# Kernel tuning notes

Hardware: AMD Instinct MI355X
Metric: run time of the kernel (lower is better)

The kernel has to match this reference:

```python
import jax, jax.numpy as jnp
import numpy as np

DIM = 1024
HIDDEN = 2816  # multiple_of * ceil(int(2*4096/3)/multiple_of)
N_MODALITIES = 2
B, S = 8, 4096


def setup_inputs() -> dict:
    key = jax.random.key(0)
    k_x, k_m, k1, k2, k3 = jax.random.split(key, 5)
    x = jax.random.normal(k_x, (B, S, DIM), dtype=jnp.float32)
    modality_ids = jax.random.randint(k_m, (B, S), 0, N_MODALITIES, dtype=jnp.int32)
    in_std = DIM ** -0.5
    out_std = HIDDEN ** -0.5
    # Linear weight layout: [out_features, in_features], stacked over modalities.
    W1 = jax.random.normal(k1, (N_MODALITIES, HIDDEN, DIM), dtype=jnp.float32) * in_std
    W3 = jax.random.normal(k3, (N_MODALITIES, HIDDEN, DIM), dtype=jnp.float32) * in_std
    W2 = jax.random.normal(k2, (N_MODALITIES, DIM, HIDDEN), dtype=jnp.float32) * out_std
    return {"x": x, "modality_ids": modality_ids, "W1": W1, "W2": W2, "W3": W3}


def reference(x, modality_ids, W1, W2, W3):
    # Masked per-modality SwiGLU; equivalent to gather -> expert MLP -> scatter.
    output = jnp.zeros_like(x)
    for m in range(N_MODALITIES):  # small fixed modality count
        mask = (modality_ids == m)[..., None]          # [B, S, 1]
        x1 = jnp.einsum('bsd,hd->bsh', x, W1[m])       # gate proj
        x3 = jnp.einsum('bsd,hd->bsh', x, W3[m])       # up proj
        out_m = jnp.einsum('bsh,dh->bsd', jax.nn.silu(x1) * x3, W2[m])
        output = output + jnp.where(mask, out_m, 0.0)
    return output
```

## Files before the change

kernel.cpp:

```cpp
#include <hip/hip_runtime.h>
#include <stdint.h>

#define DIMK 1024
#define HID  2816

typedef __attribute__((ext_vector_type(8))) __bf16 bf16x8;
typedef __attribute__((ext_vector_type(4))) float  f32x4;

typedef const __attribute__((address_space(1))) void* gas1_t;
typedef __attribute__((address_space(3))) void*       las3_t;

__device__ __forceinline__ uint16_t f2bf(float f) {
  uint32_t u = __float_as_uint(f);
  u += 0x7FFFu + ((u >> 16) & 1u);
  return (uint16_t)(u >> 16);
}

__device__ __forceinline__ void gload16(const uint16_t* g, uint16_t* l) {
  __builtin_amdgcn_global_load_lds((gas1_t)g, (las3_t)l, 16, 0, 0);
}

template<int N> __device__ __forceinline__ void wait_vm() {
  if constexpr (N == 0)      asm volatile("s_waitcnt vmcnt(0)" ::: "memory");
  else if constexpr (N == 2) asm volatile("s_waitcnt vmcnt(2)" ::: "memory");
  else                       asm volatile("s_waitcnt vmcnt(4)" ::: "memory");
}

__device__ __forceinline__ void stage_half(const uint16_t* g, long stride,
                                           uint16_t* lds, int wv, int lane) {
  const int rsub = lane >> 3;
  const int gsw  = ((lane & 7) ^ rsub) << 3;
#pragma unroll
  for (int j = 0; j < 2; ++j) {
    const int blk = j * 8 + wv;
    gload16(g + (long)(blk * 8 + rsub) * stride + gsw,
            lds + blk * 512 + lane * 8);
  }
}

__device__ __forceinline__ bf16x8 ldsf(const uint16_t* lds, int r, int g) {
  return *reinterpret_cast<const bf16x8*>(lds + r * 64 + ((g ^ (r & 7)) << 3));
}


__global__ void count_kernel(const int* __restrict__ mids, int* __restrict__ bc, int T) {
  const int b = blockIdx.x, t = threadIdx.x;
  const int token = b * 256 + t;
  const int lane = t & 63, wv = t >> 6;
  const int m = (token < T) ? mids[token] : -1;
  unsigned long long m0 = __ballot(m == 0);
  unsigned long long m1 = __ballot(m == 1);
  __shared__ int w0[4], w1[4];
  if (lane == 0) { w0[wv] = __popcll(m0); w1[wv] = __popcll(m1); }
  __syncthreads();
  if (t == 0) {
    bc[2 * b]     = w0[0] + w0[1] + w0[2] + w0[3];
    bc[2 * b + 1] = w1[0] + w1[1] + w1[2] + w1[3];
  }
}

__global__ void scan_kernel(const int* __restrict__ bc, int* __restrict__ base,
                            int* __restrict__ counters, int nb) {
  __shared__ int s0[256], s1[256];
  const int t = threadIdx.x;
  const int v0 = (t < nb) ? bc[2 * t] : 0;
  const int v1 = (t < nb) ? bc[2 * t + 1] : 0;
  s0[t] = v0; s1[t] = v1;
  __syncthreads();
  for (int off = 1; off < 256; off <<= 1) {
    int a0 = (t >= off) ? s0[t - off] : 0;
    int a1 = (t >= off) ? s1[t - off] : 0;
    __syncthreads();
    s0[t] += a0; s1[t] += a1;
    __syncthreads();
  }
  if (t < nb) { base[2 * t] = s0[t] - v0; base[2 * t + 1] = s1[t] - v1; }
  if (t == nb - 1) { counters[0] = s0[t]; counters[1] = s1[t]; }
}

__global__ void slot_kernel(const int* __restrict__ mids, const int* __restrict__ base,
                            const int* __restrict__ counters, int* __restrict__ tok,
                            int* __restrict__ slotof, int T) {
  const int b = blockIdx.x, t = threadIdx.x;
  const int token = b * 256 + t;
  const int lane = t & 63, wv = t >> 6;
  const int m = (token < T) ? mids[token] : -1;
  unsigned long long m0 = __ballot(m == 0);
  unsigned long long m1 = __ballot(m == 1);
  __shared__ int w0[4], w1[4];
  if (lane == 0) { w0[wv] = __popcll(m0); w1[wv] = __popcll(m1); }
  __syncthreads();
  int pre0 = 0, pre1 = 0;
  for (int w = 0; w < wv; ++w) { pre0 += w0[w]; pre1 += w1[w]; }
  if (token >= T) return;
  const unsigned long long below = (1ULL << lane) - 1ULL;
  const int c0 = counters[0];
  const int al0 = ((c0 + 255) >> 8) << 8;
  int slot;
  if (m == 0) slot = base[2 * b] + pre0 + __popcll(m0 & below);
  else        slot = al0 + base[2 * b + 1] + pre1 + __popcll(m1 & below);
  tok[slot] = token;
  slotof[token] = slot;
}

__global__ void copy_kernel(const float* __restrict__ x, const int* __restrict__ slotof,
                            uint16_t* __restrict__ xg, int T) {
  const int token = blockIdx.x * 4 + (threadIdx.x >> 6);
  if (token >= T) return;
  const int lane = threadIdx.x & 63;
  const int slot = slotof[token];
  const float4* src = (const float4*)(x + (long)token * DIMK);
  uint16_t* dst = xg + (long)slot * DIMK;
#pragma unroll
  for (int j = 0; j < 4; ++j) {
    float4 v = src[lane + 64 * j];
    ushort4 o;
    o.x = f2bf(v.x); o.y = f2bf(v.y); o.z = f2bf(v.z); o.w = f2bf(v.w);
    *(ushort4*)(dst + (lane + 64 * j) * 4) = o;
  }
}

__global__ void convert_kernel(const float* __restrict__ src, uint16_t* __restrict__ dst, long n) {
  long i = ((long)blockIdx.x * blockDim.x + threadIdx.x) * 4;
  if (i >= n) return;
  float4 v = *(const float4*)(src + i);
  ushort4 o;
  o.x = f2bf(v.x); o.y = f2bf(v.y); o.z = f2bf(v.z); o.w = f2bf(v.w);
  *(ushort4*)(dst + i) = o;
}


template<bool PF, int W0, int W1, int W2>
__device__ __forceinline__ void g1_tile(
    const uint16_t* Ac, const uint16_t* B1c, const uint16_t* B3c,
    uint16_t* An, uint16_t* B1n, uint16_t* B3n,
    const uint16_t* gA, const uint16_t* gB1, const uint16_t* gB3, long ko,
    int wv, int lane, int wr, int wc, int lrow, int grp,
    f32x4 (&accG)[8][2], f32x4 (&accU)[8][2]) {
  bf16x8 a[4][2], b1[2][2], b3[2][2];
  wait_vm<W0>();
  __builtin_amdgcn_s_barrier();
  asm volatile("" ::: "memory");
#pragma unroll
  for (int m = 0; m < 4; ++m)
#pragma unroll
    for (int ks = 0; ks < 2; ++ks)
      a[m][ks] = ldsf(Ac, m * 32 + wr * 16 + lrow, ks * 4 + grp);
#pragma unroll
  for (int n = 0; n < 2; ++n)
#pragma unroll
    for (int ks = 0; ks < 2; ++ks)
      b1[n][ks] = ldsf(B1c, wc * 32 + n * 16 + lrow, ks * 4 + grp);
  if constexpr (PF) stage_half(gA + ko, DIMK, An, wv, lane);
  asm volatile("s_waitcnt lgkmcnt(0)" ::: "memory");
  __builtin_amdgcn_sched_barrier(0);
  __builtin_amdgcn_s_setprio(1);
#pragma unroll
  for (int ks = 0; ks < 2; ++ks)
#pragma unroll
    for (int m = 0; m < 4; ++m)
#pragma unroll
      for (int n = 0; n < 2; ++n)
        accG[m][n] = __builtin_amdgcn_mfma_f32_16x16x32_bf16(a[m][ks], b1[n][ks], accG[m][n], 0, 0, 0);
  __builtin_amdgcn_s_setprio(0);
  wait_vm<W1>();
  __builtin_amdgcn_s_barrier();
  asm volatile("" ::: "memory");
#pragma unroll
  for (int n = 0; n < 2; ++n)
#pragma unroll
    for (int ks = 0; ks < 2; ++ks)
      b3[n][ks] = ldsf(B3c, wc * 32 + n * 16 + lrow, ks * 4 + grp);
  if constexpr (PF) stage_half(gB1 + ko, DIMK, B1n, wv, lane);
  asm volatile("s_waitcnt lgkmcnt(0)" ::: "memory");
  __builtin_amdgcn_sched_barrier(0);
  __builtin_amdgcn_s_setprio(1);
#pragma unroll
  for (int ks = 0; ks < 2; ++ks)
#pragma unroll
    for (int m = 0; m < 4; ++m)
#pragma unroll
      for (int n = 0; n < 2; ++n)
        accU[m][n] = __builtin_amdgcn_mfma_f32_16x16x32_bf16(a[m][ks], b3[n][ks], accU[m][n], 0, 0, 0);
  __builtin_amdgcn_s_setprio(0);
  wait_vm<W2>();
  __builtin_amdgcn_s_barrier();
  asm volatile("" ::: "memory");
#pragma unroll
  for (int m = 0; m < 4; ++m)
#pragma unroll
    for (int ks = 0; ks < 2; ++ks)
      a[m][ks] = ldsf(Ac, (m + 4) * 32 + wr * 16 + lrow, ks * 4 + grp);
  if constexpr (PF) stage_half(gB3 + ko, DIMK, B3n, wv, lane);
  asm volatile("s_waitcnt lgkmcnt(0)" ::: "memory");
  __builtin_amdgcn_sched_barrier(0);
  __builtin_amdgcn_s_setprio(1);
#pragma unroll
  for (int ks = 0; ks < 2; ++ks)
#pragma unroll
    for (int m = 0; m < 4; ++m)
#pragma unroll
      for (int n = 0; n < 2; ++n)
        accG[m + 4][n] = __builtin_amdgcn_mfma_f32_16x16x32_bf16(a[m][ks], b1[n][ks], accG[m + 4][n], 0, 0, 0);
  __builtin_amdgcn_s_setprio(0);
  if constexpr (PF) stage_half(gA + 128 * DIMK + ko, DIMK, An + 128 * 64, wv, lane);
  __builtin_amdgcn_s_setprio(1);
#pragma unroll
  for (int ks = 0; ks < 2; ++ks)
#pragma unroll
    for (int m = 0; m < 4; ++m)
#pragma unroll
      for (int n = 0; n < 2; ++n)
        accU[m + 4][n] = __builtin_amdgcn_mfma_f32_16x16x32_bf16(a[m][ks], b3[n][ks], accU[m + 4][n], 0, 0, 0);
  __builtin_amdgcn_s_setprio(0);
}

__global__ __launch_bounds__(512, 2) void gemm1_kernel(
    const uint16_t* __restrict__ xg, const uint16_t* __restrict__ w1b,
    const uint16_t* __restrict__ w3b, uint16_t* __restrict__ hbuf,
    const int* __restrict__ counters) {
  __shared__ __align__(16) uint16_t lsA[2][256 * 64];
  __shared__ __align__(16) uint16_t lsB1[2][128 * 64];
  __shared__ __align__(16) uint16_t lsB3[2][128 * 64];

  const int c0 = counters[0], c1 = counters[1];
  const int t0 = (c0 + 255) >> 8, t1 = (c1 + 255) >> 8;
  const int GX = gridDim.x;
  const int nwg = GX * (int)gridDim.y;
  const int orig = blockIdx.y * GX + blockIdx.x;
  const int q = nwg >> 3, r = nwg & 7;
  const int xcd = orig & 7, loc = orig >> 3;
  const int swz = (xcd < r ? xcd * (q + 1) : r * (q + 1) + (xcd - r) * q) + loc;
  const int ht = swz / GX;
  const int rt = swz - ht * GX;
  if (rt >= t0 + t1) return;
  const int mod = (rt < t0) ? 0 : 1;
  const long row0 = (long)rt * 256;

  const int tid = threadIdx.x, lane = tid & 63, wv = tid >> 6;
  const int wr = wv >> 2, wc = wv & 3;
  const int lrow = lane & 15, grp = lane >> 4;

  const uint16_t* gA  = xg  + row0 * DIMK;
  const uint16_t* gB1 = w1b + ((long)mod * HID + ht * 128) * DIMK;
  const uint16_t* gB3 = w3b + ((long)mod * HID + ht * 128) * DIMK;

  f32x4 accG[8][2], accU[8][2];
#pragma unroll
  for (int m = 0; m < 8; ++m)
#pragma unroll
    for (int n = 0; n < 2; ++n) {
      accG[m][n] = {0.f, 0.f, 0.f, 0.f};
      accU[m][n] = {0.f, 0.f, 0.f, 0.f};
    }

  stage_half(gA,             DIMK, &lsA[0][0],        wv, lane);
  stage_half(gB1,            DIMK, &lsB1[0][0],       wv, lane);
  stage_half(gB3,            DIMK, &lsB3[0][0],       wv, lane);
  stage_half(gA + 128 * DIMK, DIMK, &lsA[0][128 * 64], wv, lane);

  const int NT = DIMK / 64;
  int cur = 0;
  for (int t = 0; t < NT - 1; ++t) {
    g1_tile<true, 4, 4, 4>(&lsA[cur][0], &lsB1[cur][0], &lsB3[cur][0],
                           &lsA[cur ^ 1][0], &lsB1[cur ^ 1][0], &lsB3[cur ^ 1][0],
                           gA, gB1, gB3, (long)(t + 1) * 64,
                           wv, lane, wr, wc, lrow, grp, accG, accU);
    cur ^= 1;
  }
  g1_tile<false, 4, 2, 0>(&lsA[cur][0], &lsB1[cur][0], &lsB3[cur][0],
                          &lsA[cur ^ 1][0], &lsB1[cur ^ 1][0], &lsB3[cur ^ 1][0],
                          gA, gB1, gB3, 0,
                          wv, lane, wr, wc, lrow, grp, accG, accU);

#pragma unroll
  for (int m = 0; m < 8; ++m)
#pragma unroll
    for (int n = 0; n < 2; ++n) {
      const int col = ht * 128 + wc * 32 + n * 16 + lrow;
#pragma unroll
      for (int i = 0; i < 4; ++i) {
        const long row = row0 + m * 32 + wr * 16 + grp * 4 + i;
        float g = accG[m][n][i];
        float u = accU[m][n][i];
        float hv = (g / (1.f + __expf(-g))) * u;
        hbuf[row * HID + col] = f2bf(hv);
      }
    }
}


template<bool PF, int W0, int W1>
__device__ __forceinline__ void g2_tile(
    const uint16_t* Ac, const uint16_t* Bc, uint16_t* An, uint16_t* Bn,
    const uint16_t* gA, const uint16_t* gB, long ko,
    int wv, int lane, int wr, int wc, int lrow, int grp,
    f32x4 (&acc)[8][2]) {
  bf16x8 a[4][2], b[2][2];
  wait_vm<W0>();
  __builtin_amdgcn_s_barrier();
  asm volatile("" ::: "memory");
#pragma unroll
  for (int m = 0; m < 4; ++m)
#pragma unroll
    for (int ks = 0; ks < 2; ++ks)
      a[m][ks] = ldsf(Ac, m * 32 + wr * 16 + lrow, ks * 4 + grp);
#pragma unroll
  for (int n = 0; n < 2; ++n)
#pragma unroll
    for (int ks = 0; ks < 2; ++ks)
      b[n][ks] = ldsf(Bc, wc * 32 + n * 16 + lrow, ks * 4 + grp);
  if constexpr (PF) {
    stage_half(gA + ko, HID, An, wv, lane);
    stage_half(gB + ko, HID, Bn, wv, lane);
  }
  asm volatile("s_waitcnt lgkmcnt(0)" ::: "memory");
  __builtin_amdgcn_sched_barrier(0);
  __builtin_amdgcn_s_setprio(1);
#pragma unroll
  for (int ks = 0; ks < 2; ++ks)
#pragma unroll
    for (int m = 0; m < 4; ++m)
#pragma unroll
      for (int n = 0; n < 2; ++n)
        acc[m][n] = __builtin_amdgcn_mfma_f32_16x16x32_bf16(a[m][ks], b[n][ks], acc[m][n], 0, 0, 0);
  __builtin_amdgcn_s_setprio(0);
  wait_vm<W1>();
  __builtin_amdgcn_s_barrier();
  asm volatile("" ::: "memory");
#pragma unroll
  for (int m = 0; m < 4; ++m)
#pragma unroll
    for (int ks = 0; ks < 2; ++ks)
      a[m][ks] = ldsf(Ac, (m + 4) * 32 + wr * 16 + lrow, ks * 4 + grp);
  if constexpr (PF) stage_half(gA + 128 * HID + ko, HID, An + 128 * 64, wv, lane);
  asm volatile("s_waitcnt lgkmcnt(0)" ::: "memory");
  __builtin_amdgcn_sched_barrier(0);
  __builtin_amdgcn_s_setprio(1);
#pragma unroll
  for (int ks = 0; ks < 2; ++ks)
#pragma unroll
    for (int m = 0; m < 4; ++m)
#pragma unroll
      for (int n = 0; n < 2; ++n)
        acc[m + 4][n] = __builtin_amdgcn_mfma_f32_16x16x32_bf16(a[m][ks], b[n][ks], acc[m + 4][n], 0, 0, 0);
  __builtin_amdgcn_s_setprio(0);
}

__global__ __launch_bounds__(512, 2) void gemm2_kernel(
    const uint16_t* __restrict__ hbuf, const uint16_t* __restrict__ w2b,
    const int* __restrict__ counters, const int* __restrict__ tok,
    float* __restrict__ out) {
  __shared__ __align__(16) uint16_t lsA[2][256 * 64];
  __shared__ __align__(16) uint16_t lsB[2][128 * 64];

  const int c0 = counters[0], c1 = counters[1];
  const int t0 = (c0 + 255) >> 8, t1 = (c1 + 255) >> 8;
  const int GX = gridDim.x;
  const int nwg = GX * (int)gridDim.y;
  const int orig = blockIdx.y * GX + blockIdx.x;
  const int q = nwg >> 3, r = nwg & 7;
  const int xcd = orig & 7, loc = orig >> 3;
  const int swz = (xcd < r ? xcd * (q + 1) : r * (q + 1) + (xcd - r) * q) + loc;
  const int ct = swz / GX;
  const int rt = swz - ct * GX;
  if (rt >= t0 + t1) return;
  const int mod = (rt < t0) ? 0 : 1;
  const long row0 = (long)rt * 256;
  const int vlimit = (mod == 0) ? c0 : t0 * 256 + c1;

  const int tid = threadIdx.x, lane = tid & 63, wv = tid >> 6;
  const int wr = wv >> 2, wc = wv & 3;
  const int lrow = lane & 15, grp = lane >> 4;

  const uint16_t* gA = hbuf + row0 * HID;
  const uint16_t* gB = w2b + ((long)mod * DIMK + ct * 128) * HID;

  f32x4 acc[8][2];
#pragma unroll
  for (int m = 0; m < 8; ++m)
#pragma unroll
    for (int n = 0; n < 2; ++n) acc[m][n] = {0.f, 0.f, 0.f, 0.f};

  stage_half(gA,             HID, &lsA[0][0],        wv, lane);
  stage_half(gB,             HID, &lsB[0][0],        wv, lane);
  stage_half(gA + 128 * HID, HID, &lsA[0][128 * 64], wv, lane);

  const int NT = HID / 64;
  int cur = 0;
  for (int t = 0; t < NT - 1; ++t) {
    g2_tile<true, 2, 4>(&lsA[cur][0], &lsB[cur][0],
                        &lsA[cur ^ 1][0], &lsB[cur ^ 1][0],
                        gA, gB, (long)(t + 1) * 64,
                        wv, lane, wr, wc, lrow, grp, acc);
    cur ^= 1;
  }
  g2_tile<false, 2, 0>(&lsA[cur][0], &lsB[cur][0],
                       &lsA[cur ^ 1][0], &lsB[cur ^ 1][0],
                       gA, gB, 0,
                       wv, lane, wr, wc, lrow, grp, acc);

#pragma unroll
  for (int m = 0; m < 8; ++m)
#pragma unroll
    for (int n = 0; n < 2; ++n) {
      const int col = ct * 128 + wc * 32 + n * 16 + lrow;
#pragma unroll
      for (int i = 0; i < 4; ++i) {
        const int row = (int)row0 + m * 32 + wr * 16 + grp * 4 + i;
        if (row < vlimit) {
          out[(long)tok[row] * DIMK + col] = acc[m][n][i];
        }
      }
    }
}

extern "C" void kernel_launch(void* const* d_in, const int* in_sizes, int n_in,
                              void* d_out, int out_size, void* d_ws, size_t ws_size,
                              hipStream_t stream) {
  const float* x    = (const float*)d_in[0];
  const int*   mids = (const int*)d_in[1];
  const float* W1   = (const float*)d_in[2];
  const float* W2   = (const float*)d_in[3];
  const float* W3   = (const float*)d_in[4];
  float* out = (float*)d_out;

  const int T   = in_sizes[1];
  const int NB  = (T + 255) / 256;
  const int CAP = ((T + 255) & ~255) + 256;

  char* ws = (char*)d_ws;
  int* counters = (int*)ws;
  int* bc   = (int*)(ws + 256);
  int* base = (int*)(ws + 256 + 2048);
  int* tok  = (int*)(ws + 256 + 4096);
  int* slotof = tok + ((CAP + 63) & ~63);
  size_t off = 256 + 4096 + (size_t)((CAP + 63) & ~63) * 4 + (size_t)((T + 63) & ~63) * 4;
  off = (off + 255) & ~(size_t)255;
  uint16_t* xg  = (uint16_t*)(ws + off); off += (size_t)CAP * DIMK * 2;
  uint16_t* w1b = (uint16_t*)(ws + off); off += (size_t)2 * HID * DIMK * 2;
  uint16_t* w3b = (uint16_t*)(ws + off); off += (size_t)2 * HID * DIMK * 2;
  uint16_t* w2b = (uint16_t*)(ws + off); off += (size_t)2 * DIMK * HID * 2;
  uint16_t* hbuf = (uint16_t*)(ws + off); off += (size_t)CAP * HID * 2;
  (void)ws_size; (void)n_in; (void)out_size;

  count_kernel<<<NB, 256, 0, stream>>>(mids, bc, T);
  scan_kernel<<<1, 256, 0, stream>>>(bc, base, counters, NB);
  slot_kernel<<<NB, 256, 0, stream>>>(mids, base, counters, tok, slotof, T);
  copy_kernel<<<(T + 3) / 4, 256, 0, stream>>>(x, slotof, xg, T);

  const long NW = (long)2 * HID * DIMK;
  const int cblk = (int)((NW / 4 + 255) / 256);
  convert_kernel<<<cblk, 256, 0, stream>>>(W1, w1b, NW);
  convert_kernel<<<cblk, 256, 0, stream>>>(W3, w3b, NW);
  convert_kernel<<<cblk, 256, 0, stream>>>(W2, w2b, NW);

  const int rtiles = CAP / 256;
  gemm1_kernel<<<dim3(rtiles, HID / 128), 512, 0, stream>>>(xg, w1b, w3b, hbuf, counters);
  gemm2_kernel<<<dim3(rtiles, DIMK / 128), 512, 0, stream>>>(hbuf, w2b, counters, tok, out);
}
```

Baseline: 772.9 us.

## Widen gemm2 tile to 256 columns and restructure both GEMM inner pipelines

```diff
diff --git a/kernel.cpp b/kernel.cpp
--- a/kernel.cpp
+++ b/kernel.cpp
@@ -23,7 +23,7 @@
 template<int N> __device__ __forceinline__ void wait_vm() {
   if constexpr (N == 0)      asm volatile("s_waitcnt vmcnt(0)" ::: "memory");
   else if constexpr (N == 2) asm volatile("s_waitcnt vmcnt(2)" ::: "memory");
-  else                       asm volatile("s_waitcnt vmcnt(4)" ::: "memory");
+  else                       asm volatile("s_waitcnt vmcnt(6)" ::: "memory");
 }
 
 __device__ __forceinline__ void stage_half(const uint16_t* g, long stride,
@@ -130,7 +130,7 @@
 }
 
 
-template<bool PF, int W0, int W1, int W2>
+template<bool PF, int W0, int W2>
 __device__ __forceinline__ void g1_tile(
     const uint16_t* Ac, const uint16_t* B1c, const uint16_t* B3c,
     uint16_t* An, uint16_t* B1n, uint16_t* B3n,
@@ -143,75 +143,78 @@
   asm volatile("" ::: "memory");
 #pragma unroll
   for (int m = 0; m < 4; ++m)
-#pragma unroll
-    for (int ks = 0; ks < 2; ++ks)
-      a[m][ks] = ldsf(Ac, m * 32 + wr * 16 + lrow, ks * 4 + grp);
-#pragma unroll
-  for (int n = 0; n < 2; ++n)
-#pragma unroll
-    for (int ks = 0; ks < 2; ++ks)
-      b1[n][ks] = ldsf(B1c, wc * 32 + n * 16 + lrow, ks * 4 + grp);
-  if constexpr (PF) stage_half(gA + ko, DIMK, An, wv, lane);
-  asm volatile("s_waitcnt lgkmcnt(0)" ::: "memory");
-  __builtin_amdgcn_sched_barrier(0);
-  __builtin_amdgcn_s_setprio(1);
-#pragma unroll
-  for (int ks = 0; ks < 2; ++ks)
-#pragma unroll
-    for (int m = 0; m < 4; ++m)
-#pragma unroll
-      for (int n = 0; n < 2; ++n)
-        accG[m][n] = __builtin_amdgcn_mfma_f32_16x16x32_bf16(a[m][ks], b1[n][ks], accG[m][n], 0, 0, 0);
-  __builtin_amdgcn_s_setprio(0);
-  wait_vm<W1>();
-  __builtin_amdgcn_s_barrier();
-  asm volatile("" ::: "memory");
-#pragma unroll
-  for (int n = 0; n < 2; ++n)
-#pragma unroll
-    for (int ks = 0; ks < 2; ++ks)
-      b3[n][ks] = ldsf(B3c, wc * 32 + n * 16 + lrow, ks * 4 + grp);
-  if constexpr (PF) stage_half(gB1 + ko, DIMK, B1n, wv, lane);
-  asm volatile("s_waitcnt lgkmcnt(0)" ::: "memory");
-  __builtin_amdgcn_sched_barrier(0);
-  __builtin_amdgcn_s_setprio(1);
-#pragma unroll
-  for (int ks = 0; ks < 2; ++ks)
-#pragma unroll
-    for (int m = 0; m < 4; ++m)
-#pragma unroll
-      for (int n = 0; n < 2; ++n)
-        accU[m][n] = __builtin_amdgcn_mfma_f32_16x16x32_bf16(a[m][ks], b3[n][ks], accU[m][n], 0, 0, 0);
+    a[m][0] = ldsf(Ac, m * 32 + wr * 16 + lrow, grp);
+#pragma unroll
+  for (int n = 0; n < 2; ++n) {
+    b1[n][0] = ldsf(B1c, wc * 32 + n * 16 + lrow, grp);
+    b3[n][0] = ldsf(B3c, wc * 32 + n * 16 + lrow, grp);
+  }
+  if constexpr (PF) {
+    stage_half(gA  + ko, DIMK, An,  wv, lane);
+    stage_half(gB1 + ko, DIMK, B1n, wv, lane);
+    stage_half(gB3 + ko, DIMK, B3n, wv, lane);
+  }
+  asm volatile("s_waitcnt lgkmcnt(0)" ::: "memory");
+  __builtin_amdgcn_sched_barrier(0);
+  __builtin_amdgcn_s_setprio(1);
+#pragma unroll
+  for (int m = 0; m < 4; ++m)
+#pragma unroll
+    for (int n = 0; n < 2; ++n) {
+      accG[m][n] = __builtin_amdgcn_mfma_f32_16x16x32_bf16(a[m][0], b1[n][0], accG[m][n], 0, 0, 0);
+      accU[m][n] = __builtin_amdgcn_mfma_f32_16x16x32_bf16(a[m][0], b3[n][0], accU[m][n], 0, 0, 0);
+    }
+  __builtin_amdgcn_s_setprio(0);
+#pragma unroll
+  for (int m = 0; m < 4; ++m)
+    a[m][1] = ldsf(Ac, m * 32 + wr * 16 + lrow, 4 + grp);
+#pragma unroll
+  for (int n = 0; n < 2; ++n) {
+    b1[n][1] = ldsf(B1c, wc * 32 + n * 16 + lrow, 4 + grp);
+    b3[n][1] = ldsf(B3c, wc * 32 + n * 16 + lrow, 4 + grp);
+  }
+  asm volatile("s_waitcnt lgkmcnt(0)" ::: "memory");
+  __builtin_amdgcn_sched_barrier(0);
+  __builtin_amdgcn_s_setprio(1);
+#pragma unroll
+  for (int m = 0; m < 4; ++m)
+#pragma unroll
+    for (int n = 0; n < 2; ++n) {
+      accG[m][n] = __builtin_amdgcn_mfma_f32_16x16x32_bf16(a[m][1], b1[n][1], accG[m][n], 0, 0, 0);
+      accU[m][n] = __builtin_amdgcn_mfma_f32_16x16x32_bf16(a[m][1], b3[n][1], accU[m][n], 0, 0, 0);
+    }
   __builtin_amdgcn_s_setprio(0);
   wait_vm<W2>();
   __builtin_amdgcn_s_barrier();
   asm volatile("" ::: "memory");
 #pragma unroll
   for (int m = 0; m < 4; ++m)
-#pragma unroll
-    for (int ks = 0; ks < 2; ++ks)
-      a[m][ks] = ldsf(Ac, (m + 4) * 32 + wr * 16 + lrow, ks * 4 + grp);
-  if constexpr (PF) stage_half(gB3 + ko, DIMK, B3n, wv, lane);
-  asm volatile("s_waitcnt lgkmcnt(0)" ::: "memory");
-  __builtin_amdgcn_sched_barrier(0);
-  __builtin_amdgcn_s_setprio(1);
-#pragma unroll
-  for (int ks = 0; ks < 2; ++ks)
-#pragma unroll
-    for (int m = 0; m < 4; ++m)
-#pragma unroll
-      for (int n = 0; n < 2; ++n)
-        accG[m + 4][n] = __builtin_amdgcn_mfma_f32_16x16x32_bf16(a[m][ks], b1[n][ks], accG[m + 4][n], 0, 0, 0);
-  __builtin_amdgcn_s_setprio(0);
+    a[m][0] = ldsf(Ac, (m + 4) * 32 + wr * 16 + lrow, grp);
   if constexpr (PF) stage_half(gA + 128 * DIMK + ko, DIMK, An + 128 * 64, wv, lane);
-  __builtin_amdgcn_s_setprio(1);
-#pragma unroll
-  for (int ks = 0; ks < 2; ++ks)
-#pragma unroll
-    for (int m = 0; m < 4; ++m)
-#pragma unroll
-      for (int n = 0; n < 2; ++n)
-        accU[m + 4][n] = __builtin_amdgcn_mfma_f32_16x16x32_bf16(a[m][ks], b3[n][ks], accU[m + 4][n], 0, 0, 0);
+  asm volatile("s_waitcnt lgkmcnt(0)" ::: "memory");
+  __builtin_amdgcn_sched_barrier(0);
+  __builtin_amdgcn_s_setprio(1);
+#pragma unroll
+  for (int m = 0; m < 4; ++m)
+#pragma unroll
+    for (int n = 0; n < 2; ++n) {
+      accG[m + 4][n] = __builtin_amdgcn_mfma_f32_16x16x32_bf16(a[m][0], b1[n][0], accG[m + 4][n], 0, 0, 0);
+      accU[m + 4][n] = __builtin_amdgcn_mfma_f32_16x16x32_bf16(a[m][0], b3[n][0], accU[m + 4][n], 0, 0, 0);
+    }
+  __builtin_amdgcn_s_setprio(0);
+#pragma unroll
+  for (int m = 0; m < 4; ++m)
+    a[m][1] = ldsf(Ac, (m + 4) * 32 + wr * 16 + lrow, 4 + grp);
+  asm volatile("s_waitcnt lgkmcnt(0)" ::: "memory");
+  __builtin_amdgcn_sched_barrier(0);
+  __builtin_amdgcn_s_setprio(1);
+#pragma unroll
+  for (int m = 0; m < 4; ++m)
+#pragma unroll
+    for (int n = 0; n < 2; ++n) {
+      accG[m + 4][n] = __builtin_amdgcn_mfma_f32_16x16x32_bf16(a[m][1], b1[n][1], accG[m + 4][n], 0, 0, 0);
+      accU[m + 4][n] = __builtin_amdgcn_mfma_f32_16x16x32_bf16(a[m][1], b3[n][1], accU[m + 4][n], 0, 0, 0);
+    }
   __builtin_amdgcn_s_setprio(0);
 }
 
@@ -225,14 +228,14 @@
 
   const int c0 = counters[0], c1 = counters[1];
   const int t0 = (c0 + 255) >> 8, t1 = (c1 + 255) >> 8;
-  const int GX = gridDim.x;
-  const int nwg = GX * (int)gridDim.y;
-  const int orig = blockIdx.y * GX + blockIdx.x;
+  const int NHT = gridDim.y;
+  const int nwg = gridDim.x * NHT;
+  const int orig = blockIdx.y * gridDim.x + blockIdx.x;
   const int q = nwg >> 3, r = nwg & 7;
   const int xcd = orig & 7, loc = orig >> 3;
   const int swz = (xcd < r ? xcd * (q + 1) : r * (q + 1) + (xcd - r) * q) + loc;
-  const int ht = swz / GX;
-  const int rt = swz - ht * GX;
+  const int rt = swz / NHT;
+  const int ht = swz - rt * NHT;
   if (rt >= t0 + t1) return;
   const int mod = (rt < t0) ? 0 : 1;
   const long row0 = (long)rt * 256;
@@ -254,24 +257,24 @@
       accU[m][n] = {0.f, 0.f, 0.f, 0.f};
     }
 
-  stage_half(gA,             DIMK, &lsA[0][0],        wv, lane);
-  stage_half(gB1,            DIMK, &lsB1[0][0],       wv, lane);
-  stage_half(gB3,            DIMK, &lsB3[0][0],       wv, lane);
+  stage_half(gA,              DIMK, &lsA[0][0],        wv, lane);
+  stage_half(gB1,             DIMK, &lsB1[0][0],       wv, lane);
+  stage_half(gB3,             DIMK, &lsB3[0][0],       wv, lane);
   stage_half(gA + 128 * DIMK, DIMK, &lsA[0][128 * 64], wv, lane);
 
   const int NT = DIMK / 64;
   int cur = 0;
   for (int t = 0; t < NT - 1; ++t) {
-    g1_tile<true, 4, 4, 4>(&lsA[cur][0], &lsB1[cur][0], &lsB3[cur][0],
-                           &lsA[cur ^ 1][0], &lsB1[cur ^ 1][0], &lsB3[cur ^ 1][0],
-                           gA, gB1, gB3, (long)(t + 1) * 64,
-                           wv, lane, wr, wc, lrow, grp, accG, accU);
+    g1_tile<true, 2, 6>(&lsA[cur][0], &lsB1[cur][0], &lsB3[cur][0],
+                        &lsA[cur ^ 1][0], &lsB1[cur ^ 1][0], &lsB3[cur ^ 1][0],
+                        gA, gB1, gB3, (long)(t + 1) * 64,
+                        wv, lane, wr, wc, lrow, grp, accG, accU);
     cur ^= 1;
   }
-  g1_tile<false, 4, 2, 0>(&lsA[cur][0], &lsB1[cur][0], &lsB3[cur][0],
-                          &lsA[cur ^ 1][0], &lsB1[cur ^ 1][0], &lsB3[cur ^ 1][0],
-                          gA, gB1, gB3, 0,
-                          wv, lane, wr, wc, lrow, grp, accG, accU);
+  g1_tile<false, 2, 0>(&lsA[cur][0], &lsB1[cur][0], &lsB3[cur][0],
+                       &lsA[cur ^ 1][0], &lsB1[cur ^ 1][0], &lsB3[cur ^ 1][0],
+                       gA, gB1, gB3, 0,
+                       wv, lane, wr, wc, lrow, grp, accG, accU);
 
 #pragma unroll
   for (int m = 0; m < 8; ++m)
@@ -290,60 +293,78 @@
 }
 
 
-template<bool PF, int W0, int W1>
+template<bool PF, int W0, int W2>
 __device__ __forceinline__ void g2_tile(
     const uint16_t* Ac, const uint16_t* Bc, uint16_t* An, uint16_t* Bn,
     const uint16_t* gA, const uint16_t* gB, long ko,
     int wv, int lane, int wr, int wc, int lrow, int grp,
-    f32x4 (&acc)[8][2]) {
-  bf16x8 a[4][2], b[2][2];
+    f32x4 (&acc)[8][4]) {
+  bf16x8 a[4][2], b[4][2];
   wait_vm<W0>();
   __builtin_amdgcn_s_barrier();
   asm volatile("" ::: "memory");
 #pragma unroll
   for (int m = 0; m < 4; ++m)
-#pragma unroll
-    for (int ks = 0; ks < 2; ++ks)
-      a[m][ks] = ldsf(Ac, m * 32 + wr * 16 + lrow, ks * 4 + grp);
-#pragma unroll
-  for (int n = 0; n < 2; ++n)
-#pragma unroll
-    for (int ks = 0; ks < 2; ++ks)
-      b[n][ks] = ldsf(Bc, wc * 32 + n * 16 + lrow, ks * 4 + grp);
+    a[m][0] = ldsf(Ac, m * 32 + wr * 16 + lrow, grp);
+#pragma unroll
+  for (int n = 0; n < 4; ++n)
+    b[n][0] = ldsf(Bc, wc * 64 + n * 16 + lrow, grp);
   if constexpr (PF) {
-    stage_half(gA + ko, HID, An, wv, lane);
-    stage_half(gB + ko, HID, Bn, wv, lane);
-  }
-  asm volatile("s_waitcnt lgkmcnt(0)" ::: "memory");
-  __builtin_amdgcn_sched_barrier(0);
-  __builtin_amdgcn_s_setprio(1);
-#pragma unroll
-  for (int ks = 0; ks < 2; ++ks)
-#pragma unroll
-    for (int m = 0; m < 4; ++m)
-#pragma unroll
-      for (int n = 0; n < 2; ++n)
-        acc[m][n] = __builtin_amdgcn_mfma_f32_16x16x32_bf16(a[m][ks], b[n][ks], acc[m][n], 0, 0, 0);
-  __builtin_amdgcn_s_setprio(0);
-  wait_vm<W1>();
+    stage_half(gA + ko,             HID, An,            wv, lane);
+    stage_half(gB + ko,             HID, Bn,            wv, lane);
+    stage_half(gB + 128 * HID + ko, HID, Bn + 128 * 64, wv, lane);
+  }
+  asm volatile("s_waitcnt lgkmcnt(0)" ::: "memory");
+  __builtin_amdgcn_sched_barrier(0);
+  __builtin_amdgcn_s_setprio(1);
+#pragma unroll
+  for (int m = 0; m < 4; ++m)
+#pragma unroll
+    for (int n = 0; n < 4; ++n)
+      acc[m][n] = __builtin_amdgcn_mfma_f32_16x16x32_bf16(a[m][0], b[n][0], acc[m][n], 0, 0, 0);
+  __builtin_amdgcn_s_setprio(0);
+#pragma unroll
+  for (int m = 0; m < 4; ++m)
+    a[m][1] = ldsf(Ac, m * 32 + wr * 16 + lrow, 4 + grp);
+#pragma unroll
+  for (int n = 0; n < 4; ++n)
+    b[n][1] = ldsf(Bc, wc * 64 + n * 16 + lrow, 4 + grp);
+  asm volatile("s_waitcnt lgkmcnt(0)" ::: "memory");
+  __builtin_amdgcn_sched_barrier(0);
+  __builtin_amdgcn_s_setprio(1);
+#pragma unroll
+  for (int m = 0; m < 4; ++m)
+#pragma unroll
+    for (int n = 0; n < 4; ++n)
+      acc[m][n] = __builtin_amdgcn_mfma_f32_16x16x32_bf16(a[m][1], b[n][1], acc[m][n], 0, 0, 0);
+  __builtin_amdgcn_s_setprio(0);
+  wait_vm<W2>();
   __builtin_amdgcn_s_barrier();
   asm volatile("" ::: "memory");
 #pragma unroll
   for (int m = 0; m < 4; ++m)
-#pragma unroll
-    for (int ks = 0; ks < 2; ++ks)
-      a[m][ks] = ldsf(Ac, (m + 4) * 32 + wr * 16 + lrow, ks * 4 + grp);
+    a[m][0] = ldsf(Ac, (m + 4) * 32 + wr * 16 + lrow, grp);
   if constexpr (PF) stage_half(gA + 128 * HID + ko, HID, An + 128 * 64, wv, lane);
   asm volatile("s_waitcnt lgkmcnt(0)" ::: "memory");
   __builtin_amdgcn_sched_barrier(0);
   __builtin_amdgcn_s_setprio(1);
 #pragma unroll
-  for (int ks = 0; ks < 2; ++ks)
-#pragma unroll
-    for (int m = 0; m < 4; ++m)
-#pragma unroll
-      for (int n = 0; n < 2; ++n)
-        acc[m + 4][n] = __builtin_amdgcn_mfma_f32_16x16x32_bf16(a[m][ks], b[n][ks], acc[m + 4][n], 0, 0, 0);
+  for (int m = 0; m < 4; ++m)
+#pragma unroll
+    for (int n = 0; n < 4; ++n)
+      acc[m + 4][n] = __builtin_amdgcn_mfma_f32_16x16x32_bf16(a[m][0], b[n][0], acc[m + 4][n], 0, 0, 0);
+  __builtin_amdgcn_s_setprio(0);
+#pragma unroll
+  for (int m = 0; m < 4; ++m)
+    a[m][1] = ldsf(Ac, (m + 4) * 32 + wr * 16 + lrow, 4 + grp);
+  asm volatile("s_waitcnt lgkmcnt(0)" ::: "memory");
+  __builtin_amdgcn_sched_barrier(0);
+  __builtin_amdgcn_s_setprio(1);
+#pragma unroll
+  for (int m = 0; m < 4; ++m)
+#pragma unroll
+    for (int n = 0; n < 4; ++n)
+      acc[m + 4][n] = __builtin_amdgcn_mfma_f32_16x16x32_bf16(a[m][1], b[n][1], acc[m + 4][n], 0, 0, 0);
   __builtin_amdgcn_s_setprio(0);
 }
 
@@ -352,18 +373,18 @@
     const int* __restrict__ counters, const int* __restrict__ tok,
     float* __restrict__ out) {
   __shared__ __align__(16) uint16_t lsA[2][256 * 64];
-  __shared__ __align__(16) uint16_t lsB[2][128 * 64];
+  __shared__ __align__(16) uint16_t lsB[2][256 * 64];
 
   const int c0 = counters[0], c1 = counters[1];
   const int t0 = (c0 + 255) >> 8, t1 = (c1 + 255) >> 8;
-  const int GX = gridDim.x;
-  const int nwg = GX * (int)gridDim.y;
-  const int orig = blockIdx.y * GX + blockIdx.x;
+  const int NCT = gridDim.y;
+  const int nwg = gridDim.x * NCT;
+  const int orig = blockIdx.y * gridDim.x + blockIdx.x;
   const int q = nwg >> 3, r = nwg & 7;
   const int xcd = orig & 7, loc = orig >> 3;
   const int swz = (xcd < r ? xcd * (q + 1) : r * (q + 1) + (xcd - r) * q) + loc;
-  const int ct = swz / GX;
-  const int rt = swz - ct * GX;
+  const int rt = swz / NCT;
+  const int ct = swz - rt * NCT;
   if (rt >= t0 + t1) return;
   const int mod = (rt < t0) ? 0 : 1;
   const long row0 = (long)rt * 256;
@@ -374,22 +395,23 @@
   const int lrow = lane & 15, grp = lane >> 4;
 
   const uint16_t* gA = hbuf + row0 * HID;
-  const uint16_t* gB = w2b + ((long)mod * DIMK + ct * 128) * HID;
-
-  f32x4 acc[8][2];
+  const uint16_t* gB = w2b + ((long)mod * DIMK + ct * 256) * HID;
+
+  f32x4 acc[8][4];
 #pragma unroll
   for (int m = 0; m < 8; ++m)
 #pragma unroll
-    for (int n = 0; n < 2; ++n) acc[m][n] = {0.f, 0.f, 0.f, 0.f};
+    for (int n = 0; n < 4; ++n) acc[m][n] = {0.f, 0.f, 0.f, 0.f};
 
   stage_half(gA,             HID, &lsA[0][0],        wv, lane);
   stage_half(gB,             HID, &lsB[0][0],        wv, lane);
+  stage_half(gB + 128 * HID, HID, &lsB[0][128 * 64], wv, lane);
   stage_half(gA + 128 * HID, HID, &lsA[0][128 * 64], wv, lane);
 
   const int NT = HID / 64;
   int cur = 0;
   for (int t = 0; t < NT - 1; ++t) {
-    g2_tile<true, 2, 4>(&lsA[cur][0], &lsB[cur][0],
+    g2_tile<true, 2, 6>(&lsA[cur][0], &lsB[cur][0],
                         &lsA[cur ^ 1][0], &lsB[cur ^ 1][0],
                         gA, gB, (long)(t + 1) * 64,
                         wv, lane, wr, wc, lrow, grp, acc);
@@ -403,8 +425,8 @@
 #pragma unroll
   for (int m = 0; m < 8; ++m)
 #pragma unroll
-    for (int n = 0; n < 2; ++n) {
-      const int col = ct * 128 + wc * 32 + n * 16 + lrow;
+    for (int n = 0; n < 4; ++n) {
+      const int col = ct * 256 + wc * 64 + n * 16 + lrow;
 #pragma unroll
       for (int i = 0; i < 4; ++i) {
         const int row = (int)row0 + m * 32 + wr * 16 + grp * 4 + i;
@@ -457,5 +479,5 @@
 
   const int rtiles = CAP / 256;
   gemm1_kernel<<<dim3(rtiles, HID / 128), 512, 0, stream>>>(xg, w1b, w3b, hbuf, counters);
-  gemm2_kernel<<<dim3(rtiles, DIMK / 128), 512, 0, stream>>>(hbuf, w2b, counters, tok, out);
-}
+  gemm2_kernel<<<dim3(rtiles, DIMK / 256), 512, 0, stream>>>(hbuf, w2b, counters, tok, out);
+}
```

After: 767.2 us. About the same (-0.7%).

## Widen gemm2 output tile to 256 columns via shared two-B-panel tile routine

Applied to the files above, without the earlier changes.

```diff
diff --git a/kernel.cpp b/kernel.cpp
--- a/kernel.cpp
+++ b/kernel.cpp
@@ -23,7 +23,8 @@
 template<int N> __device__ __forceinline__ void wait_vm() {
   if constexpr (N == 0)      asm volatile("s_waitcnt vmcnt(0)" ::: "memory");
   else if constexpr (N == 2) asm volatile("s_waitcnt vmcnt(2)" ::: "memory");
-  else                       asm volatile("s_waitcnt vmcnt(4)" ::: "memory");
+  else if constexpr (N == 4) asm volatile("s_waitcnt vmcnt(4)" ::: "memory");
+  else                       asm volatile("s_waitcnt vmcnt(6)" ::: "memory");
 }
 
 __device__ __forceinline__ void stage_half(const uint16_t* g, long stride,
@@ -131,27 +132,28 @@
 
 
 template<bool PF, int W0, int W1, int W2>
-__device__ __forceinline__ void g1_tile(
-    const uint16_t* Ac, const uint16_t* B1c, const uint16_t* B3c,
-    uint16_t* An, uint16_t* B1n, uint16_t* B3n,
-    const uint16_t* gA, const uint16_t* gB1, const uint16_t* gB3, long ko,
+__device__ __forceinline__ void quad_tile(
+    const uint16_t* Ac, const uint16_t* Bxc, const uint16_t* Byc,
+    uint16_t* An, uint16_t* Bxn, uint16_t* Byn,
+    const uint16_t* gA, const uint16_t* gBx, const uint16_t* gBy,
+    long ko, long stride,
     int wv, int lane, int wr, int wc, int lrow, int grp,
-    f32x4 (&accG)[8][2], f32x4 (&accU)[8][2]) {
-  bf16x8 a[4][2], b1[2][2], b3[2][2];
+    f32x4 (&accX)[8][2], f32x4 (&accY)[8][2]) {
+  bf16x8 a[4][2], bx[2][2], by[2][2];
   wait_vm<W0>();
   __builtin_amdgcn_s_barrier();
   asm volatile("" ::: "memory");
 #pragma unroll
-  for (int m = 0; m < 4; ++m)
-#pragma unroll
-    for (int ks = 0; ks < 2; ++ks)
-      a[m][ks] = ldsf(Ac, m * 32 + wr * 16 + lrow, ks * 4 + grp);
-#pragma unroll
-  for (int n = 0; n < 2; ++n)
-#pragma unroll
-    for (int ks = 0; ks < 2; ++ks)
-      b1[n][ks] = ldsf(B1c, wc * 32 + n * 16 + lrow, ks * 4 + grp);
-  if constexpr (PF) stage_half(gA + ko, DIMK, An, wv, lane);
+  for (int m = 0; m < 4; ++m) {
+    a[m][0] = ldsf(Ac, m * 32 + wr * 16 + lrow, grp);
+    a[m][1] = ldsf(Ac, m * 32 + wr * 16 + lrow, 4 + grp);
+  }
+#pragma unroll
+  for (int n = 0; n < 2; ++n) {
+    bx[n][0] = ldsf(Bxc, wc * 32 + n * 16 + lrow, grp);
+    bx[n][1] = ldsf(Bxc, wc * 32 + n * 16 + lrow, 4 + grp);
+  }
+  if constexpr (PF) stage_half(gA + ko, stride, An, wv, lane);
   asm volatile("s_waitcnt lgkmcnt(0)" ::: "memory");
   __builtin_amdgcn_sched_barrier(0);
   __builtin_amdgcn_s_setprio(1);
@@ -161,17 +163,17 @@
     for (int m = 0; m < 4; ++m)
 #pragma unroll
       for (int n = 0; n < 2; ++n)
-        accG[m][n] = __builtin_amdgcn_mfma_f32_16x16x32_bf16(a[m][ks], b1[n][ks], accG[m][n], 0, 0, 0);
+        accX[m][n] = __builtin_amdgcn_mfma_f32_16x16x32_bf16(a[m][ks], bx[n][ks], accX[m][n], 0, 0, 0);
   __builtin_amdgcn_s_setprio(0);
   wait_vm<W1>();
   __builtin_amdgcn_s_barrier();
   asm volatile("" ::: "memory");
 #pragma unroll
-  for (int n = 0; n < 2; ++n)
-#pragma unroll
-    for (int ks = 0; ks < 2; ++ks)
-      b3[n][ks] = ldsf(B3c, wc * 32 + n * 16 + lrow, ks * 4 + grp);
-  if constexpr (PF) stage_half(gB1 + ko, DIMK, B1n, wv, lane);
+  for (int n = 0; n < 2; ++n) {
+    by[n][0] = ldsf(Byc, wc * 32 + n * 16 + lrow, grp);
+    by[n][1] = ldsf(Byc, wc * 32 + n * 16 + lrow, 4 + grp);
+  }
+  if constexpr (PF) stage_half(gBx + ko, stride, Bxn, wv, lane);
   asm volatile("s_waitcnt lgkmcnt(0)" ::: "memory");
   __builtin_amdgcn_sched_barrier(0);
   __builtin_amdgcn_s_setprio(1);
@@ -181,17 +183,17 @@
     for (int m = 0; m < 4; ++m)
 #pragma unroll
       for (int n = 0; n < 2; ++n)
-        accU[m][n] = __builtin_amdgcn_mfma_f32_16x16x32_bf16(a[m][ks], b3[n][ks], accU[m][n], 0, 0, 0);
+        accY[m][n] = __builtin_amdgcn_mfma_f32_16x16x32_bf16(a[m][ks], by[n][ks], accY[m][n], 0, 0, 0);
   __builtin_amdgcn_s_setprio(0);
   wait_vm<W2>();
   __builtin_amdgcn_s_barrier();
   asm volatile("" ::: "memory");
 #pragma unroll
-  for (int m = 0; m < 4; ++m)
-#pragma unroll
-    for (int ks = 0; ks < 2; ++ks)
-      a[m][ks] = ldsf(Ac, (m + 4) * 32 + wr * 16 + lrow, ks * 4 + grp);
-  if constexpr (PF) stage_half(gB3 + ko, DIMK, B3n, wv, lane);
+  for (int m = 0; m < 4; ++m) {
+    a[m][0] = ldsf(Ac, (m + 4) * 32 + wr * 16 + lrow, grp);
+    a[m][1] = ldsf(Ac, (m + 4) * 32 + wr * 16 + lrow, 4 + grp);
+  }
+  if constexpr (PF) stage_half(gBy + ko, stride, Byn, wv, lane);
   asm volatile("s_waitcnt lgkmcnt(0)" ::: "memory");
   __builtin_amdgcn_sched_barrier(0);
   __builtin_amdgcn_s_setprio(1);
@@ -201,9 +203,9 @@
     for (int m = 0; m < 4; ++m)
 #pragma unroll
       for (int n = 0; n < 2; ++n)
-        accG[m + 4][n] = __builtin_amdgcn_mfma_f32_16x16x32_bf16(a[m][ks], b1[n][ks], accG[m + 4][n], 0, 0, 0);
+        accX[m + 4][n] = __builtin_amdgcn_mfma_f32_16x16x32_bf16(a[m][ks], bx[n][ks], accX[m + 4][n], 0, 0, 0);
   __builtin_amdgcn_s_setprio(0);
-  if constexpr (PF) stage_half(gA + 128 * DIMK + ko, DIMK, An + 128 * 64, wv, lane);
+  if constexpr (PF) stage_half(gA + 128 * stride + ko, stride, An + 128 * 64, wv, lane);
   __builtin_amdgcn_s_setprio(1);
 #pragma unroll
   for (int ks = 0; ks < 2; ++ks)
@@ -211,9 +213,10 @@
     for (int m = 0; m < 4; ++m)
 #pragma unroll
       for (int n = 0; n < 2; ++n)
-        accU[m + 4][n] = __builtin_amdgcn_mfma_f32_16x16x32_bf16(a[m][ks], b3[n][ks], accU[m + 4][n], 0, 0, 0);
+        accY[m + 4][n] = __builtin_amdgcn_mfma_f32_16x16x32_bf16(a[m][ks], by[n][ks], accY[m + 4][n], 0, 0, 0);
   __builtin_amdgcn_s_setprio(0);
 }
+
 
 __global__ __launch_bounds__(512, 2) void gemm1_kernel(
     const uint16_t* __restrict__ xg, const uint16_t* __restrict__ w1b,
@@ -254,24 +257,24 @@
       accU[m][n] = {0.f, 0.f, 0.f, 0.f};
     }
 
-  stage_half(gA,             DIMK, &lsA[0][0],        wv, lane);
-  stage_half(gB1,            DIMK, &lsB1[0][0],       wv, lane);
-  stage_half(gB3,            DIMK, &lsB3[0][0],       wv, lane);
-  stage_half(gA + 128 * DIMK, DIMK, &lsA[0][128 * 64], wv, lane);
+  stage_half(gA,              DIMK, &lsA[0][0],         wv, lane);
+  stage_half(gB1,             DIMK, &lsB1[0][0],        wv, lane);
+  stage_half(gB3,             DIMK, &lsB3[0][0],        wv, lane);
+  stage_half(gA + 128 * DIMK, DIMK, &lsA[0][128 * 64],  wv, lane);
 
   const int NT = DIMK / 64;
   int cur = 0;
   for (int t = 0; t < NT - 1; ++t) {
-    g1_tile<true, 4, 4, 4>(&lsA[cur][0], &lsB1[cur][0], &lsB3[cur][0],
-                           &lsA[cur ^ 1][0], &lsB1[cur ^ 1][0], &lsB3[cur ^ 1][0],
-                           gA, gB1, gB3, (long)(t + 1) * 64,
-                           wv, lane, wr, wc, lrow, grp, accG, accU);
+    quad_tile<true, 4, 4, 4>(&lsA[cur][0], &lsB1[cur][0], &lsB3[cur][0],
+                             &lsA[cur ^ 1][0], &lsB1[cur ^ 1][0], &lsB3[cur ^ 1][0],
+                             gA, gB1, gB3, (long)(t + 1) * 64, DIMK,
+                             wv, lane, wr, wc, lrow, grp, accG, accU);
     cur ^= 1;
   }
-  g1_tile<false, 4, 2, 0>(&lsA[cur][0], &lsB1[cur][0], &lsB3[cur][0],
-                          &lsA[cur ^ 1][0], &lsB1[cur ^ 1][0], &lsB3[cur ^ 1][0],
-                          gA, gB1, gB3, 0,
-                          wv, lane, wr, wc, lrow, grp, accG, accU);
+  quad_tile<false, 4, 2, 0>(&lsA[cur][0], &lsB1[cur][0], &lsB3[cur][0],
+                            &lsA[cur ^ 1][0], &lsB1[cur ^ 1][0], &lsB3[cur ^ 1][0],
+                            gA, gB1, gB3, 0, DIMK,
+                            wv, lane, wr, wc, lrow, grp, accG, accU);
 
 #pragma unroll
   for (int m = 0; m < 8; ++m)
@@ -290,80 +293,24 @@
 }
 
 
-template<bool PF, int W0, int W1>
-__device__ __forceinline__ void g2_tile(
-    const uint16_t* Ac, const uint16_t* Bc, uint16_t* An, uint16_t* Bn,
-    const uint16_t* gA, const uint16_t* gB, long ko,
-    int wv, int lane, int wr, int wc, int lrow, int grp,
-    f32x4 (&acc)[8][2]) {
-  bf16x8 a[4][2], b[2][2];
-  wait_vm<W0>();
-  __builtin_amdgcn_s_barrier();
-  asm volatile("" ::: "memory");
-#pragma unroll
-  for (int m = 0; m < 4; ++m)
-#pragma unroll
-    for (int ks = 0; ks < 2; ++ks)
-      a[m][ks] = ldsf(Ac, m * 32 + wr * 16 + lrow, ks * 4 + grp);
-#pragma unroll
-  for (int n = 0; n < 2; ++n)
-#pragma unroll
-    for (int ks = 0; ks < 2; ++ks)
-      b[n][ks] = ldsf(Bc, wc * 32 + n * 16 + lrow, ks * 4 + grp);
-  if constexpr (PF) {
-    stage_half(gA + ko, HID, An, wv, lane);
-    stage_half(gB + ko, HID, Bn, wv, lane);
-  }
-  asm volatile("s_waitcnt lgkmcnt(0)" ::: "memory");
-  __builtin_amdgcn_sched_barrier(0);
-  __builtin_amdgcn_s_setprio(1);
-#pragma unroll
-  for (int ks = 0; ks < 2; ++ks)
-#pragma unroll
-    for (int m = 0; m < 4; ++m)
-#pragma unroll
-      for (int n = 0; n < 2; ++n)
-        acc[m][n] = __builtin_amdgcn_mfma_f32_16x16x32_bf16(a[m][ks], b[n][ks], acc[m][n], 0, 0, 0);
-  __builtin_amdgcn_s_setprio(0);
-  wait_vm<W1>();
-  __builtin_amdgcn_s_barrier();
-  asm volatile("" ::: "memory");
-#pragma unroll
-  for (int m = 0; m < 4; ++m)
-#pragma unroll
-    for (int ks = 0; ks < 2; ++ks)
-      a[m][ks] = ldsf(Ac, (m + 4) * 32 + wr * 16 + lrow, ks * 4 + grp);
-  if constexpr (PF) stage_half(gA + 128 * HID + ko, HID, An + 128 * 64, wv, lane);
-  asm volatile("s_waitcnt lgkmcnt(0)" ::: "memory");
-  __builtin_amdgcn_sched_barrier(0);
-  __builtin_amdgcn_s_setprio(1);
-#pragma unroll
-  for (int ks = 0; ks < 2; ++ks)
-#pragma unroll
-    for (int m = 0; m < 4; ++m)
-#pragma unroll
-      for (int n = 0; n < 2; ++n)
-        acc[m + 4][n] = __builtin_amdgcn_mfma_f32_16x16x32_bf16(a[m][ks], b[n][ks], acc[m + 4][n], 0, 0, 0);
-  __builtin_amdgcn_s_setprio(0);
-}
-
 __global__ __launch_bounds__(512, 2) void gemm2_kernel(
     const uint16_t* __restrict__ hbuf, const uint16_t* __restrict__ w2b,
     const int* __restrict__ counters, const int* __restrict__ tok,
     float* __restrict__ out) {
   __shared__ __align__(16) uint16_t lsA[2][256 * 64];
-  __shared__ __align__(16) uint16_t lsB[2][128 * 64];
+  __shared__ __align__(16) uint16_t lsBx[2][128 * 64];
+  __shared__ __align__(16) uint16_t lsBy[2][128 * 64];
 
   const int c0 = counters[0], c1 = counters[1];
   const int t0 = (c0 + 255) >> 8, t1 = (c1 + 255) >> 8;
-  const int GX = gridDim.x;
-  const int nwg = GX * (int)gridDim.y;
-  const int orig = blockIdx.y * GX + blockIdx.x;
+  const int NCT = gridDim.y;
+  const int nwg = gridDim.x * NCT;
+  const int orig = blockIdx.y * gridDim.x + blockIdx.x;
   const int q = nwg >> 3, r = nwg & 7;
   const int xcd = orig & 7, loc = orig >> 3;
   const int swz = (xcd < r ? xcd * (q + 1) : r * (q + 1) + (xcd - r) * q) + loc;
-  const int ct = swz / GX;
-  const int rt = swz - ct * GX;
+  const int rt = swz / NCT;
+  const int ct = swz - rt * NCT;
   if (rt >= t0 + t1) return;
   const int mod = (rt < t0) ? 0 : 1;
   const long row0 = (long)rt * 256;
@@ -373,43 +320,50 @@
   const int wr = wv >> 2, wc = wv & 3;
   const int lrow = lane & 15, grp = lane >> 4;
 
-  const uint16_t* gA = hbuf + row0 * HID;
-  const uint16_t* gB = w2b + ((long)mod * DIMK + ct * 128) * HID;
-
-  f32x4 acc[8][2];
+  const uint16_t* gA  = hbuf + row0 * HID;
+  const uint16_t* gBx = w2b + ((long)mod * DIMK + ct * 256) * HID;
+  const uint16_t* gBy = gBx + 128 * HID;
+
+  f32x4 accX[8][2], accY[8][2];
 #pragma unroll
   for (int m = 0; m < 8; ++m)
 #pragma unroll
-    for (int n = 0; n < 2; ++n) acc[m][n] = {0.f, 0.f, 0.f, 0.f};
+    for (int n = 0; n < 2; ++n) {
+      accX[m][n] = {0.f, 0.f, 0.f, 0.f};
+      accY[m][n] = {0.f, 0.f, 0.f, 0.f};
+    }
 
   stage_half(gA,             HID, &lsA[0][0],        wv, lane);
-  stage_half(gB,             HID, &lsB[0][0],        wv, lane);
+  stage_half(gBx,            HID, &lsBx[0][0],       wv, lane);
+  stage_half(gBy,            HID, &lsBy[0][0],       wv, lane);
   stage_half(gA + 128 * HID, HID, &lsA[0][128 * 64], wv, lane);
 
   const int NT = HID / 64;
   int cur = 0;
   for (int t = 0; t < NT - 1; ++t) {
-    g2_tile<true, 2, 4>(&lsA[cur][0], &lsB[cur][0],
-                        &lsA[cur ^ 1][0], &lsB[cur ^ 1][0],
-                        gA, gB, (long)(t + 1) * 64,
-                        wv, lane, wr, wc, lrow, grp, acc);
+    quad_tile<true, 4, 4, 4>(&lsA[cur][0], &lsBx[cur][0], &lsBy[cur][0],
+                             &lsA[cur ^ 1][0], &lsBx[cur ^ 1][0], &lsBy[cur ^ 1][0],
+                             gA, gBx, gBy, (long)(t + 1) * 64, HID,
+                             wv, lane, wr, wc, lrow, grp, accX, accY);
     cur ^= 1;
   }
-  g2_tile<false, 2, 0>(&lsA[cur][0], &lsB[cur][0],
-                       &lsA[cur ^ 1][0], &lsB[cur ^ 1][0],
-                       gA, gB, 0,
-                       wv, lane, wr, wc, lrow, grp, acc);
+  quad_tile<false, 4, 2, 0>(&lsA[cur][0], &lsBx[cur][0], &lsBy[cur][0],
+                            &lsA[cur ^ 1][0], &lsBx[cur ^ 1][0], &lsBy[cur ^ 1][0],
+                            gA, gBx, gBy, 0, HID,
+                            wv, lane, wr, wc, lrow, grp, accX, accY);
 
 #pragma unroll
   for (int m = 0; m < 8; ++m)
 #pragma unroll
     for (int n = 0; n < 2; ++n) {
-      const int col = ct * 128 + wc * 32 + n * 16 + lrow;
+      const int colX = ct * 256 + wc * 32 + n * 16 + lrow;
 #pragma unroll
       for (int i = 0; i < 4; ++i) {
         const int row = (int)row0 + m * 32 + wr * 16 + grp * 4 + i;
         if (row < vlimit) {
-          out[(long)tok[row] * DIMK + col] = acc[m][n][i];
+          const long obase = (long)tok[row] * DIMK;
+          out[obase + colX]       = accX[m][n][i];
+          out[obase + colX + 128] = accY[m][n][i];
         }
       }
     }
@@ -457,5 +411,5 @@
 
   const int rtiles = CAP / 256;
   gemm1_kernel<<<dim3(rtiles, HID / 128), 512, 0, stream>>>(xg, w1b, w3b, hbuf, counters);
-  gemm2_kernel<<<dim3(rtiles, DIMK / 128), 512, 0, stream>>>(hbuf, w2b, counters, tok, out);
-}
+  gemm2_kernel<<<dim3(rtiles, DIMK / 256), 512, 0, stream>>>(hbuf, w2b, counters, tok, out);
+}
```

Result: faster. 706.1 us (-8.6%).
